# Kernel tuning notes

Measured on AMD Instinct MI355X. Metric: run time of the kernel, lower is better.

The kernel has to match this reference:

```python
import jax, jax.numpy as jnp
import numpy as np


def setup_inputs() -> dict:
    key = jax.random.key(0)
    k1, k2, k3, k4 = jax.random.split(key, 4)
    B, N, D, P = 1, 8192, 128, 2  # batch must be 1 (see .view(B,N,N) in source)
    x = jax.random.normal(k1, (B, N, D), dtype=jnp.float32)
    points = jax.random.normal(k2, (B, N, P), dtype=jnp.float32)
    # nn.Linear params, stored as (in, out) so y = x @ W + b
    W1 = jax.random.normal(k3, (2 * D, 2 * D), dtype=jnp.float32) * 0.04
    b1 = jnp.zeros((2 * D,), dtype=jnp.float32)
    W2 = jax.random.normal(k4, (2 * D, D), dtype=jnp.float32) * 0.04
    b2 = jnp.zeros((D,), dtype=jnp.float32)
    return {"x": x, "points": points, "W1": W1, "b1": b1, "W2": W2, "b2": b2, "K": 16}


def reference(x, points, W1, b1, W2, b2, K):
    B, N, _ = points.shape
    D = x.shape[-1]
    # torch.cdist on flattened (B*N, P) points, reshaped to (B, N, N)
    # (valid only for B == 1, matching the original module). Squared distance
    # is monotone in Euclidean distance, so top-k indices are identical.
    pf = points.reshape(B * N, -1)
    sq = jnp.sum(pf * pf, axis=-1)
    d2 = sq[:, None] + sq[None, :] - 2.0 * (pf @ pf.T)  # (BN, BN)
    d2 = d2.reshape(B, N, N)
    # topk(-dist, K+1) -> nearest K+1 (self first), drop self
    _, idx = jax.lax.top_k(-d2, K + 1)  # (B, N, K+1)
    idx = idx[:, :, 1:]  # (B, N, K)
    # gather neighbor features: knn_fts[b, n, k] = x[b, idx[b, n, k]]
    knn = x[jnp.arange(B)[:, None, None], idx]  # (B, N, K, D)
    center = jnp.broadcast_to(x[:, :, None, :], (B, N, K, D))
    local = jnp.concatenate([knn - center, center], axis=-1)  # (B, N, K, 2D)
    h = jax.nn.gelu(local @ W1 + b1, approximate=False)
    h = jax.nn.gelu(h @ W2 + b2, approximate=False)
    return jnp.mean(h, axis=2)  # (B, N, D)
```

## Files before the change

### kernel.cpp

```cpp
#include <hip/hip_runtime.h>

typedef __attribute__((ext_vector_type(8))) short short8;
typedef __attribute__((ext_vector_type(4))) float f32x4;

__device__ __forceinline__ unsigned short f2bf(float f) {
    unsigned int u = __float_as_uint(f);
    unsigned int r = u + 0x7fffu + ((u >> 16) & 1u);
    return (unsigned short)(r >> 16);
}

__device__ __forceinline__ float bf2f(short s) {
    return __uint_as_float(((unsigned int)(unsigned short)s) << 16);
}

__device__ __forceinline__ float gelu_fast(float v) {
    float x2 = v * v;
    float s  = v * fmaf(-0.102943195f, x2, -2.3022077f);
    float e  = __builtin_amdgcn_exp2f(s);
    return v * __builtin_amdgcn_rcpf(1.0f + e);
}

__device__ __forceinline__ unsigned int d2key(float d2) {
    unsigned int u = __float_as_uint(d2);
    return u ^ (((unsigned int)(((int)u) >> 31)) | 0x80000000u);
}

#define U64MAX 0xFFFFFFFFFFFFFFFFull

#define D2_FROM_Q(px, py, XI, YI, SQI)                                           \
    ({ const float sqj_ = __fadd_rn(__fmul_rn((px), (px)), __fmul_rn((py), (py))); \
       const float t_   = fmaf((YI), (py), __fmul_rn((XI), (px)));                 \
       const float s_   = __fadd_rn((SQI), sqj_);                                  \
       fmaf(-2.0f, t_, s_); })

__device__ __forceinline__ unsigned long long bitonic64(unsigned long long v, int lane) {
#pragma unroll
    for (int k = 2; k <= 64; k <<= 1) {
#pragma unroll
        for (int j = k >> 1; j > 0; j >>= 1) {
            unsigned long long pv = __shfl_xor(v, j, 64);
            const bool up  = ((lane & k) == 0);
            const bool low = ((lane & j) == 0);
            const unsigned long long mn = (v < pv) ? v : pv;
            const unsigned long long mx = (v < pv) ? pv : v;
            v = (up == low) ? mn : mx;
        }
    }
    return v;
}

__device__ __forceinline__ float bitonic64f(float v, int lane) {
#pragma unroll
    for (int k = 2; k <= 64; k <<= 1) {
#pragma unroll
        for (int j = k >> 1; j > 0; j >>= 1) {
            float pv = __shfl_xor(v, j, 64);
            const bool up  = ((lane & k) == 0);
            const bool low = ((lane & j) == 0);
            const float mn = fminf(v, pv);
            const float mx = fmaxf(v, pv);
            v = (up == low) ? mn : mx;
        }
    }
    return v;
}

__device__ __forceinline__ void insert_cand(
        unsigned long long* crow, int* cnt,
        float px, float py, float XI, float YI, float SQI, int i) {
    const float d2 = D2_FROM_Q(px, py, XI, YI, SQI);
    const unsigned int key = d2key(d2);
    int pos = atomicAdd(cnt, 1);
    if (pos < 128)
        crow[pos] = ((unsigned long long)key << 32) | (unsigned int)i;
}

#define KNN_SLACK 2.0e-3f

__global__ __launch_bounds__(256) void knn_kernel(
        const float* __restrict__ points,
        const float* __restrict__ W1, const float* __restrict__ W2,
        unsigned short* __restrict__ W1t, unsigned short* __restrict__ W2t,
        int* __restrict__ idx_out) {
    __shared__ unsigned long long cand[16][128];
    __shared__ int ccnt[16];

    const int bid = blockIdx.x;
    const int tid = threadIdx.x;

    if (bid < 384) {
        int g = bid * 256 + tid;
        if (g < 65536) {
            int d = g >> 8, c = g & 255;
            W1t[c * 256 + d] = f2bf(W1[g]);
        } else if (g < 98304) {
            int g2 = g - 65536;
            int d = g2 >> 7, c = g2 & 127;
            W2t[c * 256 + d] = f2bf(W2[g2]);
        }
        return;
    }

    const int wv    = tid >> 6;
    const int lane  = tid & 63;
    const int qbase = ((bid - 384) << 4) | (wv << 2);

    float xi[4], yi[4], sqi_[4], n2x[4], n2y[4];
#pragma unroll
    for (int t = 0; t < 4; ++t) {
        xi[t] = points[(qbase + t) * 2 + 0];
        yi[t] = points[(qbase + t) * 2 + 1];
        sqi_[t] = __fadd_rn(__fmul_rn(xi[t], xi[t]), __fmul_rn(yi[t], yi[t]));
        n2x[t] = -2.0f * xi[t];
        n2y[t] = -2.0f * yi[t];
    }

    const float4* p4 = (const float4*)points;

    if (lane < 4) ccnt[(wv << 2) + lane] = 0;

    float vmn[4] = {1e30f, 1e30f, 1e30f, 1e30f};
#pragma unroll 8
    for (int j = 0; j < 64; ++j) {
        const float4 pp = p4[j * 64 + lane];
        const float sqa = fmaf(pp.x, pp.x, pp.y * pp.y);
        const float sqb = fmaf(pp.z, pp.z, pp.w * pp.w);
#pragma unroll
        for (int t = 0; t < 4; ++t) {
            const float da = fmaf(n2x[t], pp.x, fmaf(n2y[t], pp.y, sqa));
            const float db = fmaf(n2x[t], pp.z, fmaf(n2y[t], pp.w, sqb));
            vmn[t] = fminf(fminf(da, db), vmn[t]);
        }
    }

    float Ta[4];
#pragma unroll
    for (int t = 0; t < 4; ++t) {
        const float s = bitonic64f(vmn[t], lane);
        Ta[t] = __shfl(s, 16, 64) + KNN_SLACK;
    }

    __syncthreads();

#pragma unroll 4
    for (int j = 0; j < 64; ++j) {
        const float4 pp = p4[j * 64 + lane];
        const int i0 = j * 128 + lane * 2;
        const float sqa = fmaf(pp.x, pp.x, pp.y * pp.y);
        const float sqb = fmaf(pp.z, pp.z, pp.w * pp.w);
#pragma unroll
        for (int t = 0; t < 4; ++t) {
            const float da = fmaf(n2x[t], pp.x, fmaf(n2y[t], pp.y, sqa));
            const float db = fmaf(n2x[t], pp.z, fmaf(n2y[t], pp.w, sqb));
            if (da <= Ta[t])
                insert_cand(cand[(wv << 2) + t], &ccnt[(wv << 2) + t],
                            pp.x, pp.y, xi[t], yi[t], sqi_[t], i0);
            if (db <= Ta[t])
                insert_cand(cand[(wv << 2) + t], &ccnt[(wv << 2) + t],
                            pp.z, pp.w, xi[t], yi[t], sqi_[t], i0 + 1);
        }
    }
    __syncthreads();

#pragma unroll 1
    for (int qi = 0; qi < 4; ++qi) {
        const int q = qbase + qi;
        unsigned long long* candw = cand[(wv << 2) + qi];
        const int cc = ccnt[(wv << 2) + qi];
        const int n = cc < 128 ? cc : 128;
        if (n <= 64) {
            unsigned long long v0 = (lane < n) ? candw[lane] : U64MAX;
            v0 = bitonic64(v0, lane);
            if (lane >= 1 && lane <= 16)
                idx_out[q * 16 + lane - 1] = (int)(unsigned int)(v0 & 0xFFFFFFFFull);
        } else {
            unsigned long long v0 = (lane < n)      ? candw[lane]      : U64MAX;
            unsigned long long v1 = (lane + 64 < n) ? candw[lane + 64] : U64MAX;
#pragma unroll 1
            for (int pick = 0; pick < 17; ++pick) {
                unsigned long long m = (v0 < v1) ? v0 : v1;
#pragma unroll
                for (int d = 1; d < 64; d <<= 1) {
                    unsigned long long pm = __shfl_xor(m, d, 64);
                    m = (pm < m) ? pm : m;
                }
                if (pick > 0 && lane == 0)
                    idx_out[q * 16 + pick - 1] = (int)(unsigned int)(m & 0xFFFFFFFFull);
                if (v0 == m) v0 = U64MAX;
                else if (v1 == m) v1 = U64MAX;
            }
        }
    }
}

__global__ __launch_bounds__(256) void gemmAD_kernel(
        const float* __restrict__ x, const unsigned short* __restrict__ W1t,
        const float* __restrict__ b1,
        unsigned short* __restrict__ Abf, unsigned short* __restrict__ Dbf) {
    __shared__ unsigned short sx[64 * 136];
    const int tid = threadIdx.x;
    const int rb  = (blockIdx.x >> 1) * 64;
    const int cb  = (blockIdx.x & 1) * 128;

    {
        const int r   = ((tid >> 6) << 4) | (tid & 15);
        const int seg = (tid >> 4) & 3;
        const float* xr = x + (rb + r) * 128 + seg * 32;
        unsigned short* dst = sx + r * 136 + seg * 32;
#pragma unroll
        for (int u = 0; u < 8; ++u) {
            float4 a = ((const float4*)xr)[u];
            uint2 w;
            w.x = (unsigned)f2bf(a.x) | ((unsigned)f2bf(a.y) << 16);
            w.y = (unsigned)f2bf(a.z) | ((unsigned)f2bf(a.w) << 16);
            *(uint2*)(dst + u * 4) = w;
        }
    }
    __syncthreads();

    const int lane = tid & 63, wv = tid >> 6;
    const int m = lane & 15, quad = lane >> 4;
    const int ko0 = quad * 8;

    f32x4 accA[8], accC[8];
#pragma unroll
    for (int i = 0; i < 8; ++i) { accA[i] = (f32x4){0,0,0,0}; accC[i] = (f32x4){0,0,0,0}; }

#pragma unroll
    for (int ks = 0; ks < 4; ++ks) {
        const int ko = ks * 32 + ko0;
        short8 af[4], bA[2], bC[2];
#pragma unroll
        for (int rt = 0; rt < 4; ++rt)
            af[rt] = *(const short8*)(sx + (rt * 16 + m) * 136 + ko);
#pragma unroll
        for (int ct = 0; ct < 2; ++ct) {
            const unsigned short* wp = W1t + (cb + wv * 32 + ct * 16 + m) * 256 + ko;
            bA[ct] = *(const short8*)(wp);
            bC[ct] = *(const short8*)(wp + 128);
        }
#pragma unroll
        for (int rt = 0; rt < 4; ++rt)
#pragma unroll
            for (int ct = 0; ct < 2; ++ct) {
                accA[rt * 2 + ct] = __builtin_amdgcn_mfma_f32_16x16x32_bf16(
                    af[rt], bA[ct], accA[rt * 2 + ct], 0, 0, 0);
                accC[rt * 2 + ct] = __builtin_amdgcn_mfma_f32_16x16x32_bf16(
                    af[rt], bC[ct], accC[rt * 2 + ct], 0, 0, 0);
            }
    }

#pragma unroll
    for (int ct = 0; ct < 2; ++ct) {
        const int col = cb + wv * 32 + ct * 16 + m;
        const float bias = b1[col];
#pragma unroll
        for (int rt = 0; rt < 4; ++rt)
#pragma unroll
            for (int j = 0; j < 4; ++j) {
                const int row = rb + rt * 16 + quad * 4 + j;
                float a = accA[rt * 2 + ct][j];
                float d = accC[rt * 2 + ct][j] - a + bias;
                Abf[row * 256 + col] = f2bf(a);
                Dbf[row * 256 + col] = f2bf(d);
            }
    }
}

__global__ __launch_bounds__(256) void mlp_kernel(
        const unsigned short* __restrict__ Abf, const unsigned short* __restrict__ Dbf,
        const unsigned short* __restrict__ W2t, const float* __restrict__ b2,
        const int* __restrict__ idx, float* __restrict__ out) {
    __shared__ unsigned short sh[64 * 264];
    const int tid = threadIdx.x;
    const int qb  = blockIdx.x << 2;

    {
        const int r   = ((tid >> 6) << 4) | (tid & 15);
        const int seg = (tid >> 4) & 3;
        const int gq  = qb + (r >> 4);
        const int nb  = idx[(gq << 4) + (r & 15)];
        const unsigned short* arow = Abf + nb * 256 + seg * 64;
        const unsigned short* drow = Dbf + gq * 256 + seg * 64;
        unsigned short* dst = sh + r * 264 + seg * 64;
#pragma unroll
        for (int u = 0; u < 8; ++u) {
            short8 av = *(const short8*)(arow + u * 8);
            short8 dv = *(const short8*)(drow + u * 8);
            short8 hv;
#pragma unroll
            for (int e = 0; e < 8; ++e) {
                float h = bf2f(av[e]) + bf2f(dv[e]);
                hv[e] = (short)f2bf(gelu_fast(h));
            }
            *(short8*)(dst + u * 8) = hv;
        }
    }
    __syncthreads();

    const int lane = tid & 63, wv = tid >> 6;
    const int m = lane & 15, quad = lane >> 4;
    const int ko0 = quad * 8;

    f32x4 acc2[8];
#pragma unroll
    for (int i = 0; i < 8; ++i) acc2[i] = (f32x4){0.f, 0.f, 0.f, 0.f};
#pragma unroll
    for (int ks = 0; ks < 8; ++ks) {
        const int ko = ks * 32 + ko0;
        short8 af[4], bfr[2];
#pragma unroll
        for (int rt = 0; rt < 4; ++rt)
            af[rt] = *(const short8*)(sh + (rt * 16 + m) * 264 + ko);
#pragma unroll
        for (int ct = 0; ct < 2; ++ct)
            bfr[ct] = *(const short8*)(W2t + (wv * 32 + ct * 16 + m) * 256 + ko);
#pragma unroll
        for (int rt = 0; rt < 4; ++rt)
#pragma unroll
            for (int ct = 0; ct < 2; ++ct)
                acc2[rt * 2 + ct] = __builtin_amdgcn_mfma_f32_16x16x32_bf16(
                    af[rt], bfr[ct], acc2[rt * 2 + ct], 0, 0, 0);
    }

#pragma unroll
    for (int ct = 0; ct < 2; ++ct) {
        const int col = wv * 32 + ct * 16 + m;
        const float bias = b2[col];
#pragma unroll
        for (int rt = 0; rt < 4; ++rt) {
            float s = 0.f;
#pragma unroll
            for (int j = 0; j < 4; ++j)
                s += gelu_fast(acc2[rt * 2 + ct][j] + bias);
            s += __shfl_xor(s, 16, 64);
            s += __shfl_xor(s, 32, 64);
            if (quad == 0) out[(qb + rt) * 128 + col] = s * 0.0625f;
        }
    }
}

extern "C" void kernel_launch(void* const* d_in, const int* in_sizes, int n_in,
                              void* d_out, int out_size, void* d_ws, size_t ws_size,
                              hipStream_t stream) {
    const float* x      = (const float*)d_in[0];
    const float* points = (const float*)d_in[1];
    const float* W1     = (const float*)d_in[2];
    const float* b1     = (const float*)d_in[3];
    const float* W2     = (const float*)d_in[4];
    const float* b2     = (const float*)d_in[5];
    float* out = (float*)d_out;

    char* ws = (char*)d_ws;
    unsigned short* W1t = (unsigned short*)ws;
    unsigned short* W2t = (unsigned short*)(ws + 131072);
    int*            idx = (int*)(ws + 196608);
    unsigned short* Abf = (unsigned short*)(ws + 720896);
    unsigned short* Dbf = (unsigned short*)(ws + 4915200);

    knn_kernel<<<896, 256, 0, stream>>>(points, W1, W2, W1t, W2t, idx);
    gemmAD_kernel<<<256, 256, 0, stream>>>(x, W1t, b1, Abf, Dbf);
    mlp_kernel<<<2048, 256, 0, stream>>>(Abf, Dbf, W2t, b2, idx, out);
}
```

Baseline: 149.8 us.

## Split kNN candidate scan across four waves per query group

Each block now handles 4 queries instead of 16, and its four waves each scan a quarter of the point set for those queries rather than one wave scanning all points. Per-wave partial minima are merged through shared memory to form the per-query threshold, candidates go into shared per-query lists, and each wave then selects top-k for one query. This cuts the serial scan length per wave and launches more blocks for better latency hiding. The cost is extra syncthreads and more shared-memory atomic contention on the candidate counters.

```diff
diff --git a/kernel.cpp b/kernel.cpp
--- a/kernel.cpp
+++ b/kernel.cpp
@@ -82,8 +82,10 @@
         const float* __restrict__ W1, const float* __restrict__ W2,
         unsigned short* __restrict__ W1t, unsigned short* __restrict__ W2t,
         int* __restrict__ idx_out) {
-    __shared__ unsigned long long cand[16][128];
-    __shared__ int ccnt[16];
+    __shared__ float pmin[4][4][64];
+    __shared__ float tshr[4];
+    __shared__ unsigned long long cand[4][128];
+    __shared__ int ccnt[4];
 
     const int bid = blockIdx.x;
     const int tid = threadIdx.x;
@@ -103,7 +105,7 @@
 
     const int wv    = tid >> 6;
     const int lane  = tid & 63;
-    const int qbase = ((bid - 384) << 4) | (wv << 2);
+    const int qbase = (bid - 384) << 2;
 
     float xi[4], yi[4], sqi_[4], n2x[4], n2y[4];
 #pragma unroll
@@ -116,13 +118,14 @@
     }
 
     const float4* p4 = (const float4*)points;
-
-    if (lane < 4) ccnt[(wv << 2) + lane] = 0;
+    const float4* pw = p4 + wv * 1024 + lane;
+
+    if (tid < 4) ccnt[tid] = 0;
 
     float vmn[4] = {1e30f, 1e30f, 1e30f, 1e30f};
-#pragma unroll 8
-    for (int j = 0; j < 64; ++j) {
-        const float4 pp = p4[j * 64 + lane];
+#pragma unroll 4
+    for (int j = 0; j < 16; ++j) {
+        const float4 pp = pw[j * 64];
         const float sqa = fmaf(pp.x, pp.x, pp.y * pp.y);
         const float sqb = fmaf(pp.z, pp.z, pp.w * pp.w);
 #pragma unroll
@@ -132,20 +135,26 @@
             vmn[t] = fminf(fminf(da, db), vmn[t]);
         }
     }
-
+#pragma unroll
+    for (int t = 0; t < 4; ++t) pmin[t][wv][lane] = vmn[t];
+    __syncthreads();
+
+    {
+        const int q = wv;
+        const float m = fminf(fminf(pmin[q][0][lane], pmin[q][1][lane]),
+                              fminf(pmin[q][2][lane], pmin[q][3][lane]));
+        const float s = bitonic64f(m, lane);
+        if (lane == 16) tshr[q] = s + KNN_SLACK;
+    }
+    __syncthreads();
     float Ta[4];
 #pragma unroll
-    for (int t = 0; t < 4; ++t) {
-        const float s = bitonic64f(vmn[t], lane);
-        Ta[t] = __shfl(s, 16, 64) + KNN_SLACK;
-    }
-
-    __syncthreads();
+    for (int t = 0; t < 4; ++t) Ta[t] = tshr[t];
 
 #pragma unroll 4
-    for (int j = 0; j < 64; ++j) {
-        const float4 pp = p4[j * 64 + lane];
-        const int i0 = j * 128 + lane * 2;
+    for (int j = 0; j < 16; ++j) {
+        const float4 pp = pw[j * 64];
+        const int i0 = (wv * 1024 + j * 64 + lane) * 2;
         const float sqa = fmaf(pp.x, pp.x, pp.y * pp.y);
         const float sqb = fmaf(pp.z, pp.z, pp.w * pp.w);
 #pragma unroll
@@ -153,20 +162,19 @@
             const float da = fmaf(n2x[t], pp.x, fmaf(n2y[t], pp.y, sqa));
             const float db = fmaf(n2x[t], pp.z, fmaf(n2y[t], pp.w, sqb));
             if (da <= Ta[t])
-                insert_cand(cand[(wv << 2) + t], &ccnt[(wv << 2) + t],
+                insert_cand(cand[t], &ccnt[t],
                             pp.x, pp.y, xi[t], yi[t], sqi_[t], i0);
             if (db <= Ta[t])
-                insert_cand(cand[(wv << 2) + t], &ccnt[(wv << 2) + t],
+                insert_cand(cand[t], &ccnt[t],
                             pp.z, pp.w, xi[t], yi[t], sqi_[t], i0 + 1);
         }
     }
     __syncthreads();
 
-#pragma unroll 1
-    for (int qi = 0; qi < 4; ++qi) {
-        const int q = qbase + qi;
-        unsigned long long* candw = cand[(wv << 2) + qi];
-        const int cc = ccnt[(wv << 2) + qi];
+    {
+        const int q = qbase + wv;
+        unsigned long long* candw = cand[wv];
+        const int cc = ccnt[wv];
         const int n = cc < 128 ? cc : 128;
         if (n <= 64) {
             unsigned long long v0 = (lane < n) ? candw[lane] : U64MAX;
@@ -358,7 +366,7 @@
     unsigned short* Abf = (unsigned short*)(ws + 720896);
     unsigned short* Dbf = (unsigned short*)(ws + 4915200);
 
-    knn_kernel<<<896, 256, 0, stream>>>(points, W1, W2, W1t, W2t, idx);
+    knn_kernel<<<2432, 256, 0, stream>>>(points, W1, W2, W1t, W2t, idx);
     gemmAD_kernel<<<256, 256, 0, stream>>>(x, W1t, b1, Abf, Dbf);
     mlp_kernel<<<2048, 256, 0, stream>>>(Abf, Dbf, W2t, b2, idx, out);
 }
```

Result: faster. 131.4 us (-12.3%).
